# Optimization experiments

Measured on AMD Instinct MI355X. Metric: run time of the kernel, lower is better.

## Reference

```python
import jax, jax.numpy as jnp
import numpy as np

NUM_HEADS = 4
D_K = 64
D_MODEL = NUM_HEADS * D_K  # 256
SEN_LEN = 8192
N_GROUPS = 4096
BASE_LEN = 64
N_EDGES = N_GROUPS * BASE_LEN  # 262144
PATH_LEN = 64


def setup_inputs() -> dict:
    rng = np.random.default_rng(0)
    key = jax.random.key(0)
    ks = jax.random.split(key, 16)

    # ragged group lengths, each >= 2, summing exactly to N_EDGES
    half = N_GROUPS // 2
    r = rng.integers(-(BASE_LEN - 2), BASE_LEN - 1, size=half)
    edge_len = np.concatenate([BASE_LEN + r, BASE_LEN - r]).astype(np.int64)
    assert edge_len.sum() == N_EDGES and edge_len.min() >= 2

    # distinct token ids; include src=0 and tar=1 so path_agg branches fire
    perm = rng.permutation(np.arange(2, SEN_LEN))[: N_GROUPS - 2]
    token_ids = np.concatenate([np.array([0, 1]), perm]).astype(np.int64)

    def w(k, shape):
        return jax.random.normal(k, shape, jnp.float32) / np.sqrt(shape[-1]).astype(np.float32)

    return {
        "path": jax.random.normal(ks[0], (PATH_LEN, D_MODEL), jnp.float32),
        "path_len": PATH_LEN,
        "q": jax.random.normal(ks[1], (SEN_LEN, D_MODEL), jnp.float32),
        "k": jax.random.normal(ks[2], (N_EDGES, D_MODEL), jnp.float32),
        "v": jax.random.normal(ks[3], (N_EDGES, D_MODEL), jnp.float32),
        "graphs": 0,
        "edge_len": jnp.asarray(edge_len),
        "token_ids": jnp.asarray(token_ids),
        "pair": jnp.array([0, 1], jnp.int32),
        "rev": 0,
        "W_qpair": w(ks[4], (D_MODEL, 2 * D_MODEL)),
        "W_pk": w(ks[5], (D_MODEL, D_MODEL)),
        "W_pv": w(ks[6], (D_MODEL, D_MODEL)),
        "W_q": w(ks[7], (D_MODEL, D_MODEL)),
        "W_k": w(ks[8], (D_MODEL, D_MODEL)),
        "W_v": w(ks[9], (D_MODEL, D_MODEL)),
        "W_out": w(ks[10], (D_MODEL, D_MODEL)),
        "b_out": jnp.zeros((D_MODEL,), jnp.float32),
        "W_agg": w(ks[11], (D_MODEL, 2 * D_MODEL)),
    }


def _forward(path, q, k, v, edge_len, token_ids, pair, rev,
             W_qpair, W_pk, W_pv, W_q, W_k, W_v, W_out, b_out, W_agg):
    H, dk = NUM_HEADS, D_K
    G = edge_len.shape[0]
    E = k.shape[0]
    scale = 1.0 / jnp.sqrt(jnp.float32(dk))

    src = pair[0] if rev == 0 else pair[1]
    tar = pair[1] if rev == 0 else pair[0]

    # pair query: cat(q[src], q[tar]) -> linear -> [H, 1, dk]
    pair_q = (jnp.concatenate([q[src], q[tar]]) @ W_qpair.T).reshape(1, H, dk).transpose(1, 0, 2)

    qh = (q @ W_q.T).reshape(-1, H, dk).transpose(1, 0, 2)      # [H, S, dk]
    pk = (path @ W_pk.T).reshape(-1, H, dk).transpose(1, 0, 2)  # [H, P, dk]
    pv = (path @ W_pv.T).reshape(-1, H, dk).transpose(1, 0, 2)  # [H, P, dk]
    kh = (k @ W_k.T).reshape(-1, H, dk).transpose(1, 0, 2)      # [H, E, dk]
    vh = (v @ W_v.T).reshape(-1, H, dk).transpose(1, 0, 2)      # [H, E, dk]

    # ---- pair/path attention ----
    att = jax.nn.softmax(jnp.einsum('hqd,hpd->hqp', pair_q, pk) * scale, axis=-1)  # [H,1,P]
    path_vals = jnp.einsum('hqp,hpd->hqd', att, pv).sum(axis=1)  # [H, dk]
    path_result = path_vals.reshape(-1) @ W_out.T + b_out        # [d_model]

    # ---- segmented per-group attention (vectorized ragged loop) ----
    seg = jnp.repeat(jnp.arange(G), edge_len, total_repeat_length=E)  # [E]
    q_sel = qh[:, token_ids, :]          # [H, G, dk] query per group
    qe = q_sel[:, seg, :]                # [H, E, dk] query per edge
    # torch.matmul(q_[H,dk], k_[H,i,dk].T) broadcasts to cross-head logits [a,b,i]
    logits = jnp.einsum('aed,bed->eab', qe, kh) * scale  # [E, H, H]
    lmax = jax.lax.stop_gradient(jax.ops.segment_max(logits, seg, num_segments=G))
    ex = jnp.exp(logits - lmax[seg])
    denom = jax.ops.segment_sum(ex, seg, num_segments=G)
    p = ex / denom[seg]                                   # segmented softmax [E, H, H]
    # sum over key-head b per edge, then segment-reduce over edges of each group
    out_e = jnp.einsum('eab,bed->ead', p, vh)             # [E, H, dk]
    hid = jax.ops.segment_sum(out_e, seg, num_segments=G) # [G, H, dk]
    new_hid = hid.reshape(G, H * dk) @ W_out.T + b_out    # [G, d_model] (dropout=identity)

    # ---- assemble output rows ----
    pr = jnp.broadcast_to(path_result, (G, D_MODEL))
    feat_path = jnp.concatenate([new_hid, pr], axis=1) @ W_agg.T  # token == src
    path_feat = jnp.concatenate([pr, new_hid], axis=1) @ W_agg.T  # token == tar
    is_src = (token_ids == src)[:, None]
    is_tar = (token_ids == tar)[:, None]
    vals = jnp.where(is_src, feat_path, jnp.where(is_tar, path_feat, new_hid))
    returned = q.at[token_ids].set(vals)
    return returned, att


def reference(path, path_len, q, k, v, graphs, edge_len, token_ids, pair, rev,
              W_qpair, W_pk, W_pv, W_q, W_k, W_v, W_out, b_out, W_agg):
    return _forward(path, q, k, v, edge_len, token_ids, pair, rev,
                    W_qpair, W_pk, W_pv, W_q, W_k, W_v, W_out, b_out, W_agg)
```

## Files before the change

### kernel.cpp

```cpp
#include <hip/hip_runtime.h>
#include <hip/hip_bf16.h>

#define H 4
#define DK 64
#define DM 256
#define SEN 8192
#define NG 4096
#define ETOT 262144
#define PLEN 64
#define MAXE 128

typedef unsigned short ushortT;
typedef __attribute__((ext_vector_type(8))) __bf16 bf16x8;
typedef __attribute__((ext_vector_type(8))) unsigned short us8;
typedef __attribute__((ext_vector_type(4))) unsigned short us4;
typedef __attribute__((ext_vector_type(4))) float f32x4;

#define TMS 264

__device__ __forceinline__ ushortT f2bf(float f) {
    unsigned u = __float_as_uint(f);
    u += 0x7FFF + ((u >> 16) & 1);
    return (ushortT)(u >> 16);
}

__device__ __forceinline__ bf16x8 ldb8(const ushortT* p) {
    us8 v = *(const us8*)p;
    return __builtin_bit_cast(bf16x8, v);
}

__device__ __forceinline__ bf16x8 pack8(const float* f) {
    us8 v;
#pragma unroll
    for (int j = 0; j < 8; j++) v[j] = f2bf(f[j]);
    return __builtin_bit_cast(bf16x8, v);
}

__global__ __launch_bounds__(256) void scan_kernel(const int* __restrict__ edge_len,
                                                   int* __restrict__ starts) {
    __shared__ int part[256];
    const int tid = threadIdx.x;
    const int base = tid * 16;
    int loc[16];
    int s = 0;
#pragma unroll
    for (int i = 0; i < 16; i++) { loc[i] = s; s += edge_len[base + i]; }
    part[tid] = s;
    __syncthreads();
    if (tid == 0) {
        int acc = 0;
        for (int i = 0; i < 256; i++) { int t = part[i]; part[i] = acc; acc += t; }
    }
    __syncthreads();
    const int off = part[tid];
#pragma unroll
    for (int i = 0; i < 16; i++) starts[base + i] = off + loc[i];
}

__global__ void copy_kernel(const float* __restrict__ q, float* __restrict__ out) {
    const size_t i = (size_t)blockIdx.x * blockDim.x + threadIdx.x;
    ((float4*)out)[i] = ((const float4*)q)[i];
}

__global__ __launch_bounds__(256) void wprep_kernel(
    const float* __restrict__ W_q, const float* __restrict__ W_k,
    const float* __restrict__ W_v, const float* __restrict__ W_out,
    ushortT* __restrict__ WQb, ushortT* __restrict__ WKTb,
    ushortT* __restrict__ WVb, ushortT* __restrict__ WOb) {
    const int idx = blockIdx.x * 256 + threadIdx.x;
    const int sel = idx >> 16;
    const int i = idx & 65535;
    if (sel == 0) {
        WQb[i] = f2bf(W_q[i]);
    } else if (sel == 1) {
        const int c = i >> 8, d = i & 255;
        WKTb[i] = f2bf(W_k[d * DM + c]);
    } else if (sel == 2) {
        WVb[i] = f2bf(W_v[i]);
    } else {
        WOb[i] = f2bf(W_out[i]);
    }
}

__global__ __launch_bounds__(256) void qh_kernel(
    const float* __restrict__ q, const int* __restrict__ token_ids,
    const ushortT* __restrict__ WQb, ushortT* __restrict__ QHb) {
    __shared__ ushortT Al[64 * 264];
    const int tid = threadIdx.x;
    const int g0 = blockIdx.x * 64;
    {
        const int m = tid >> 2;
        const int c0 = (tid & 3) * 64;
        const int tok = token_ids[g0 + m];
        const float* qr = &q[(size_t)tok * DM + c0];
#pragma unroll
        for (int i = 0; i < 16; i++) {
            float4 v4 = *(const float4*)&qr[i * 4];
            us4 o;
            o[0] = f2bf(v4.x); o[1] = f2bf(v4.y); o[2] = f2bf(v4.z); o[3] = f2bf(v4.w);
            *(us4*)&Al[m * 264 + c0 + i * 4] = o;
        }
    }
    __syncthreads();
    const int lane = tid & 63, w = tid >> 6, lq = lane & 15, lh = lane >> 4;
    bf16x8 af[8];
#pragma unroll
    for (int kk = 0; kk < 8; kk++)
        af[kk] = ldb8(&Al[(w * 16 + lq) * 264 + kk * 32 + lh * 8]);
    for (int nt = 0; nt < 16; nt++) {
        f32x4 acc = {0.f, 0.f, 0.f, 0.f};
#pragma unroll
        for (int kk = 0; kk < 8; kk++) {
            bf16x8 bf = ldb8(&WQb[(nt * 16 + lq) * 256 + kk * 32 + lh * 8]);
            acc = __builtin_amdgcn_mfma_f32_16x16x32_bf16(af[kk], bf, acc, 0, 0, 0);
        }
#pragma unroll
        for (int r = 0; r < 4; r++)
            QHb[(size_t)(g0 + w * 16 + lh * 4 + r) * 256 + nt * 16 + lq] = f2bf(acc[r]);
    }
}

__global__ __launch_bounds__(256) void tmat_kernel(
    const ushortT* __restrict__ QHb, const ushortT* __restrict__ WKTb,
    ushortT* __restrict__ tmat_u) {
    const int tid = threadIdx.x;
    const int g0 = blockIdx.x * 64;
    const int ab = blockIdx.y;
    const int a = ab >> 2, b = ab & 3;
    const int lane = tid & 63, w = tid >> 6, lq = lane & 15, lh = lane >> 4;
    bf16x8 a0 = ldb8(&QHb[(size_t)(g0 + w * 16 + lq) * 256 + a * 64 + lh * 8]);
    bf16x8 a1 = ldb8(&QHb[(size_t)(g0 + w * 16 + lq) * 256 + a * 64 + 32 + lh * 8]);
    for (int nt = 0; nt < 16; nt++) {
        f32x4 acc = {0.f, 0.f, 0.f, 0.f};
        bf16x8 b0 = ldb8(&WKTb[(nt * 16 + lq) * 256 + b * 64 + lh * 8]);
        acc = __builtin_amdgcn_mfma_f32_16x16x32_bf16(a0, b0, acc, 0, 0, 0);
        bf16x8 b1 = ldb8(&WKTb[(nt * 16 + lq) * 256 + b * 64 + 32 + lh * 8]);
        acc = __builtin_amdgcn_mfma_f32_16x16x32_bf16(a1, b1, acc, 0, 0, 0);
#pragma unroll
        for (int r = 0; r < 4; r++)
            tmat_u[((size_t)(g0 + w * 16 + lh * 4 + r) * 16 + ab) * 256 + nt * 16 + lq] =
                f2bf(acc[r]);
    }
}

__global__ __launch_bounds__(256) void edge_kernel(
    const float* __restrict__ k, const float* __restrict__ v,
    const int* __restrict__ edge_len, const int* __restrict__ starts,
    ushortT* __restrict__ tmat_u) {
    const int g = blockIdx.x;
    const int tid = threadIdx.x;
    const float scale = 0.125f;
    __shared__ float plog[128][17];
    __shared__ ushortT pT[16 * 136];
    __shared__ float red[16][16];
    __shared__ float mx[16];
    const int start = starts[g];
    const int len = edge_len[g];
    const int lane = tid & 63, w = tid >> 6, lq = lane & 15, lh = lane >> 4;
    const int rg = tid >> 4, cc = tid & 15;

    bf16x8 btm[8];
#pragma unroll
    for (int cb = 0; cb < 8; cb++)
        btm[cb] = ldb8(&tmat_u[((size_t)g * 16 + lq) * 256 + cb * 32 + lh * 8]);

    const int nmt = (len + 15) >> 4;
    for (int t = w; t < nmt; t += 4) {
        const int e = t * 16 + lq;
        const int ec = (e < len) ? e : (len - 1);
        const float* krow = &k[(size_t)(start + ec) * DM + lh * 8];
        f32x4 acc = {0.f, 0.f, 0.f, 0.f};
#pragma unroll
        for (int cb = 0; cb < 8; cb++) {
            float4 k0 = *(const float4*)&krow[cb * 32];
            float4 k1 = *(const float4*)&krow[cb * 32 + 4];
            float kf[8] = {k0.x, k0.y, k0.z, k0.w, k1.x, k1.y, k1.z, k1.w};
            acc = __builtin_amdgcn_mfma_f32_16x16x32_bf16(pack8(kf), btm[cb], acc, 0, 0, 0);
        }
#pragma unroll
        for (int r = 0; r < 4; r++) plog[t * 16 + lh * 4 + r][lq] = acc[r] * scale;
    }
    __syncthreads();

    const int nkc = (len + 31) >> 5;
    {
        float m = -3.0e38f;
        for (int e = rg; e < len; e += 16) m = fmaxf(m, plog[e][cc]);
        red[rg][cc] = m;
        __syncthreads();
        if (tid < 16) {
            float mm = red[0][tid];
            for (int i2 = 1; i2 < 16; i2++) mm = fmaxf(mm, red[i2][tid]);
            mx[tid] = mm;
        }
        __syncthreads();
        const float mm = mx[cc];
        float s = 0.f;
        for (int e = rg; e < len; e += 16) {
            float ex = __expf(plog[e][cc] - mm);
            plog[e][cc] = ex;
            s += ex;
        }
        red[rg][cc] = s;
        __syncthreads();
        if (tid < 16) {
            float ss = red[0][tid];
            for (int i2 = 1; i2 < 16; i2++) ss += red[i2][tid];
            mx[tid] = 1.0f / ss;
        }
        __syncthreads();
        const float inv = mx[cc];
        const int padlen = nkc * 32;
        for (int e = rg; e < padlen; e += 16) {
            float pv = (e < len) ? plog[e][cc] * inv : 0.f;
            pT[cc * 136 + e] = f2bf(pv);
        }
    }
    __syncthreads();

    {
        f32x4 uacc[4];
#pragma unroll
        for (int nt = 0; nt < 4; nt++) uacc[nt] = {0.f, 0.f, 0.f, 0.f};
        const int c0 = w * 64;
#pragma unroll
        for (int kc = 0; kc < 4; kc++) {
            if (kc < nkc) {
                bf16x8 ap = ldb8(&pT[lq * 136 + kc * 32 + lh * 8]);
#pragma unroll
                for (int nt = 0; nt < 4; nt++) {
                    float bf[8];
#pragma unroll
                    for (int j = 0; j < 8; j++) {
                        int e = kc * 32 + lh * 8 + j;
                        int ecl = (e < len) ? e : (len - 1);
                        bf[j] = v[(size_t)(start + ecl) * DM + c0 + nt * 16 + lq];
                    }
                    uacc[nt] = __builtin_amdgcn_mfma_f32_16x16x32_bf16(ap, pack8(bf), uacc[nt], 0, 0, 0);
                }
            }
        }
#pragma unroll
        for (int nt = 0; nt < 4; nt++) {
#pragma unroll
            for (int r = 0; r < 4; r++) {
                const int ab = lh * 4 + r;
                tmat_u[((size_t)g * 16 + ab) * 256 + c0 + nt * 16 + lq] = f2bf(uacc[nt][r]);
            }
        }
    }
}

__global__ __launch_bounds__(256) void hid_kernel(
    const ushortT* __restrict__ Ub, const ushortT* __restrict__ WVb,
    ushortT* __restrict__ HIDb) {
    const int tid = threadIdx.x;
    const int g0 = blockIdx.x * 64;
    const int a = blockIdx.y;
    const int lane = tid & 63, w = tid >> 6, lq = lane & 15, lh = lane >> 4;
    f32x4 acc[4];
#pragma unroll
    for (int nt = 0; nt < 4; nt++) acc[nt] = {0.f, 0.f, 0.f, 0.f};
    for (int kk = 0; kk < 32; kk++) {
        const int kbase = kk * 32 + lh * 8;
        bf16x8 af = ldb8(&Ub[((size_t)(g0 + w * 16 + lq) * 16 + a * 4) * 256 + kbase]);
#pragma unroll
        for (int nt = 0; nt < 4; nt++) {
            bf16x8 bf = ldb8(&WVb[(size_t)((kbase >> 8) * 64 + nt * 16 + lq) * 256 + (kbase & 255)]);
            acc[nt] = __builtin_amdgcn_mfma_f32_16x16x32_bf16(af, bf, acc[nt], 0, 0, 0);
        }
    }
#pragma unroll
    for (int nt = 0; nt < 4; nt++) {
#pragma unroll
        for (int r = 0; r < 4; r++)
            HIDb[(size_t)(g0 + w * 16 + lh * 4 + r) * 256 + a * 64 + nt * 16 + lq] =
                f2bf(acc[nt][r]);
    }
}

__global__ __launch_bounds__(256) void nh_kernel(
    const ushortT* __restrict__ HIDb, const ushortT* __restrict__ WOb,
    const float* __restrict__ b_out, const int* __restrict__ token_ids,
    float* __restrict__ nh_ws, float* __restrict__ out) {
    const int tid = threadIdx.x;
    const int g0 = blockIdx.x * 64;
    const int lane = tid & 63, w = tid >> 6, lq = lane & 15, lh = lane >> 4;
    bf16x8 af[8];
#pragma unroll
    for (int kk = 0; kk < 8; kk++)
        af[kk] = ldb8(&HIDb[(size_t)(g0 + w * 16 + lq) * 256 + kk * 32 + lh * 8]);
    int toks[4];
#pragma unroll
    for (int r = 0; r < 4; r++) toks[r] = token_ids[g0 + w * 16 + lh * 4 + r];
    for (int nt = 0; nt < 16; nt++) {
        f32x4 acc = {0.f, 0.f, 0.f, 0.f};
#pragma unroll
        for (int kk = 0; kk < 8; kk++) {
            bf16x8 bf = ldb8(&WOb[(nt * 16 + lq) * 256 + kk * 32 + lh * 8]);
            acc = __builtin_amdgcn_mfma_f32_16x16x32_bf16(af[kk], bf, acc, 0, 0, 0);
        }
        const int n = nt * 16 + lq;
        const float bo = b_out[n];
#pragma unroll
        for (int r = 0; r < 4; r++) {
            const int g = g0 + w * 16 + lh * 4 + r;
            const float val = acc[r] + bo;
            nh_ws[(size_t)g * 256 + n] = val;
            out[(size_t)toks[r] * DM + n] = val;
        }
    }
}

__global__ __launch_bounds__(256) void agg_kernel(
    const int* __restrict__ token_ids, const int* __restrict__ pair,
    const int* __restrict__ rev, const float* __restrict__ W_agg,
    const float* __restrict__ path_result, const float* __restrict__ nh_ws,
    float* __restrict__ out) {
    __shared__ int gsrc, gtar;
    __shared__ float catS[512], catT[512];
    const int tid = threadIdx.x;
    if (tid == 0) { gsrc = -1; gtar = -1; }
    __syncthreads();
    const int rv = rev[0];
    const int src = (rv == 0) ? pair[0] : pair[1];
    const int tar = (rv == 0) ? pair[1] : pair[0];
    for (int i = tid; i < NG; i += 256) {
        const int tk = token_ids[i];
        if (tk == src) gsrc = i;
        if (tk == tar) gtar = i;
    }
    __syncthreads();
    const int gs = gsrc, gt = gtar;
    if (gs >= 0) {
        catS[tid] = nh_ws[(size_t)gs * 256 + tid];
        catS[256 + tid] = path_result[tid];
    }
    if (gt >= 0) {
        catT[tid] = path_result[tid];
        catT[256 + tid] = nh_ws[(size_t)gt * 256 + tid];
    }
    __syncthreads();
    if (gs >= 0) {
        float acc = 0.f;
        for (int n = 0; n < 512; n += 4) {
            float4 w4 = *(const float4*)&W_agg[(size_t)tid * 512 + n];
            acc += w4.x * catS[n] + w4.y * catS[n + 1] + w4.z * catS[n + 2] + w4.w * catS[n + 3];
        }
        out[(size_t)src * DM + tid] = acc;
    }
    if (gt >= 0) {
        float acc = 0.f;
        for (int n = 0; n < 512; n += 4) {
            float4 w4 = *(const float4*)&W_agg[(size_t)tid * 512 + n];
            acc += w4.x * catT[n] + w4.y * catT[n + 1] + w4.z * catT[n + 2] + w4.w * catT[n + 3];
        }
        out[(size_t)tar * DM + tid] = acc;
    }
}

__global__ __launch_bounds__(256) void pathB_kernel(
    const float* __restrict__ path, const float* __restrict__ q,
    const int* __restrict__ pair, const int* __restrict__ rev,
    const float* __restrict__ W_qpair, const float* __restrict__ W_pk,
    const float* __restrict__ W_pv,
    float* __restrict__ pv_ws, float* __restrict__ logits_ws) {
    __shared__ float cat[512];
    __shared__ float pq[256];
    __shared__ float prow[256];
    __shared__ float lp[256];
    const int p = blockIdx.x;
    const int tid = threadIdx.x;
    const int rv = rev[0];
    const int src = (rv == 0) ? pair[0] : pair[1];
    const int tar = (rv == 0) ? pair[1] : pair[0];
    cat[tid] = q[(size_t)src * DM + tid];
    cat[256 + tid] = q[(size_t)tar * DM + tid];
    prow[tid] = path[p * DM + tid];
    __syncthreads();
    float acc = 0.f;
    for (int c = 0; c < 512; c += 4) {
        float4 w4 = *(const float4*)&W_qpair[(size_t)tid * 512 + c];
        acc += w4.x * cat[c] + w4.y * cat[c + 1] + w4.z * cat[c + 2] + w4.w * cat[c + 3];
    }
    pq[tid] = acc;
    __syncthreads();
    float pkv = 0.f, pvv = 0.f;
    for (int c = 0; c < 256; c += 4) {
        float4 a4 = *(const float4*)&W_pk[tid * DM + c];
        float4 b4 = *(const float4*)&W_pv[tid * DM + c];
        float4 x4 = *(const float4*)&prow[c];
        pkv += a4.x * x4.x + a4.y * x4.y + a4.z * x4.z + a4.w * x4.w;
        pvv += b4.x * x4.x + b4.y * x4.y + b4.z * x4.z + b4.w * x4.w;
    }
    pv_ws[p * DM + tid] = pvv;
    lp[tid] = pq[tid] * pkv;
    __syncthreads();
    if (tid < H) {
        float s = 0.f;
        for (int d = 0; d < DK; d++) s += lp[tid * DK + d];
        logits_ws[tid * PLEN + p] = s * 0.125f;
    }
}

__global__ __launch_bounds__(256) void pathC_kernel(
    const float* __restrict__ pv_ws, const float* __restrict__ logits_ws,
    const float* __restrict__ W_out, const float* __restrict__ b_out,
    float* __restrict__ att_out, float* __restrict__ path_result) {
    __shared__ float att[256];
    __shared__ float pvals[256];
    const int tid = threadIdx.x;
    att[tid] = logits_ws[tid];
    __syncthreads();
    if (tid < H) {
        float m = -3.0e38f;
        for (int p = 0; p < PLEN; p++) m = fmaxf(m, att[tid * PLEN + p]);
        float s = 0.f;
        for (int p = 0; p < PLEN; p++) {
            float e = __expf(att[tid * PLEN + p] - m);
            att[tid * PLEN + p] = e;
            s += e;
        }
        float inv = 1.f / s;
        for (int p = 0; p < PLEN; p++) att[tid * PLEN + p] *= inv;
    }
    __syncthreads();
    att_out[tid] = att[tid];
    {
        const int h = tid >> 6;
        float a = 0.f;
        for (int p = 0; p < PLEN; p++) a += att[h * PLEN + p] * pv_ws[p * DM + tid];
        pvals[tid] = a;
    }
    __syncthreads();
    {
        float a = b_out[tid];
        for (int c = 0; c < 256; c += 4) {
            float4 w4 = *(const float4*)&W_out[tid * DM + c];
            a += w4.x * pvals[c] + w4.y * pvals[c + 1] + w4.z * pvals[c + 2] + w4.w * pvals[c + 3];
        }
        path_result[tid] = a;
    }
}

__global__ __launch_bounds__(256, 4) void group_kernel(
    const float* __restrict__ q, const float* __restrict__ k, const float* __restrict__ v,
    const int* __restrict__ edge_len, const int* __restrict__ token_ids,
    const int* __restrict__ pair, const int* __restrict__ rev,
    const float* __restrict__ W_q,
    const float* __restrict__ W_k, const float* __restrict__ W_v,
    const float* __restrict__ W_out, const float* __restrict__ b_out,
    const float* __restrict__ W_agg,
    const int* __restrict__ starts, const float* __restrict__ path_result,
    float* __restrict__ out) {
    const int g = blockIdx.x;
    const int tid = threadIdx.x;
    const float scale = 0.125f;

    __shared__ float qrow[256];
    __shared__ float qh[256];
    __shared__ ushortT qh_b[4 * 72];
    __shared__ ushortT tmat_b[16 * TMS];
    __shared__ float plog[128][17];
    __shared__ ushortT pT[16 * 136];
    __shared__ ushortT u_b[4 * 1032];
    __shared__ float hid[256];
    __shared__ float nh[256];
    __shared__ float red[16][16];
    __shared__ float mx[16];

    const int tok = token_ids[g];
    const int start = starts[g];
    const int len = edge_len[g];

    const int lane = tid & 63;
    const int w = tid >> 6;
    const int lq = lane & 15;
    const int lh = lane >> 4;
    const int rg = tid >> 4;
    const int cc = tid & 15;

    qrow[tid] = q[(size_t)tok * DM + tid];
    __syncthreads();

    for (int i = 0; i < 16; i++) {
        const int r = i * 16 + rg;
        float acc = 0.f;
#pragma unroll
        for (int j4 = 0; j4 < 4; j4++) {
            const int c0 = j4 * 64 + cc * 4;
            float4 w4 = *(const float4*)&W_q[r * DM + c0];
            float4 x4 = *(const float4*)&qrow[c0];
            acc += w4.x * x4.x + w4.y * x4.y + w4.z * x4.z + w4.w * x4.w;
        }
#pragma unroll
        for (int off = 8; off; off >>= 1) acc += __shfl_down(acc, off, 16);
        if (cc == 0) qh[r] = acc;
    }
    __syncthreads();
    qh_b[(tid >> 6) * 72 + (tid & 63)] = f2bf(qh[tid]);
    __syncthreads();

    {
        const int arow = (lq < 3) ? lq : 3;
        bf16x8 aq0 = ldb8(&qh_b[arow * 72 + lh * 8]);
        bf16x8 aq1 = ldb8(&qh_b[arow * 72 + 32 + lh * 8]);
        for (int nt = 0; nt < 16; nt++) {
            const int c = nt * 16 + lq;
            f32x4 acc = {0.f, 0.f, 0.f, 0.f};
            float wf[8];
#pragma unroll
            for (int j = 0; j < 8; j++)
                wf[j] = W_k[(size_t)(w * 64 + lh * 8 + j) * DM + c];
            acc = __builtin_amdgcn_mfma_f32_16x16x32_bf16(aq0, pack8(wf), acc, 0, 0, 0);
#pragma unroll
            for (int j = 0; j < 8; j++)
                wf[j] = W_k[(size_t)(w * 64 + 32 + lh * 8 + j) * DM + c];
            acc = __builtin_amdgcn_mfma_f32_16x16x32_bf16(aq1, pack8(wf), acc, 0, 0, 0);
            if (lane < 16) {
#pragma unroll
                for (int r = 0; r < 4; r++)
                    tmat_b[(r * 4 + w) * TMS + nt * 16 + lq] = f2bf(acc[r]);
            }
        }
    }
    __syncthreads();

    {
        bf16x8 btm[8];
#pragma unroll
        for (int cb = 0; cb < 8; cb++)
            btm[cb] = ldb8(&tmat_b[lq * TMS + cb * 32 + lh * 8]);
        const int nmt = (len + 15) >> 4;
        for (int t = w; t < nmt; t += 4) {
            const int e = t * 16 + lq;
            const int ec = (e < len) ? e : (len - 1);
            const float* krow = &k[(size_t)(start + ec) * DM + lh * 8];
            f32x4 acc = {0.f, 0.f, 0.f, 0.f};
#pragma unroll
            for (int cb = 0; cb < 8; cb++) {
                float4 k0 = *(const float4*)&krow[cb * 32];
                float4 k1 = *(const float4*)&krow[cb * 32 + 4];
                float kf[8] = {k0.x, k0.y, k0.z, k0.w, k1.x, k1.y, k1.z, k1.w};
                acc = __builtin_amdgcn_mfma_f32_16x16x32_bf16(pack8(kf), btm[cb], acc, 0, 0, 0);
            }
#pragma unroll
            for (int r = 0; r < 4; r++) plog[t * 16 + lh * 4 + r][lq] = acc[r] * scale;
        }
    }
    __syncthreads();

    const int nkc = (len + 31) >> 5;
    {
        float m = -3.0e38f;
        for (int e = rg; e < len; e += 16) m = fmaxf(m, plog[e][cc]);
        red[rg][cc] = m;
        __syncthreads();
        if (tid < 16) {
            float mm = red[0][tid];
            for (int i2 = 1; i2 < 16; i2++) mm = fmaxf(mm, red[i2][tid]);
            mx[tid] = mm;
        }
        __syncthreads();
        const float mm = mx[cc];
        float s = 0.f;
        for (int e = rg; e < len; e += 16) {
            float ex = __expf(plog[e][cc] - mm);
            plog[e][cc] = ex;
            s += ex;
        }
        red[rg][cc] = s;
        __syncthreads();
        if (tid < 16) {
            float ss = red[0][tid];
            for (int i2 = 1; i2 < 16; i2++) ss += red[i2][tid];
            mx[tid] = 1.0f / ss;
        }
        __syncthreads();
        const float inv = mx[cc];
        const int padlen = nkc * 32;
        for (int e = rg; e < padlen; e += 16) {
            float pv = (e < len) ? plog[e][cc] * inv : 0.f;
            pT[cc * 136 + e] = f2bf(pv);
        }
    }
    __syncthreads();

    {
        f32x4 uacc[4];
#pragma unroll
        for (int nt = 0; nt < 4; nt++) uacc[nt] = {0.f, 0.f, 0.f, 0.f};
        const int c0 = w * 64;
#pragma unroll
        for (int kc = 0; kc < 4; kc++) {
            if (kc < nkc) {
                bf16x8 ap = ldb8(&pT[lq * 136 + kc * 32 + lh * 8]);
#pragma unroll
                for (int nt = 0; nt < 4; nt++) {
                    float bf[8];
#pragma unroll
                    for (int j = 0; j < 8; j++) {
                        int e = kc * 32 + lh * 8 + j;
                        int ecl = (e < len) ? e : (len - 1);
                        bf[j] = v[(size_t)(start + ecl) * DM + c0 + nt * 16 + lq];
                    }
                    uacc[nt] = __builtin_amdgcn_mfma_f32_16x16x32_bf16(ap, pack8(bf), uacc[nt], 0, 0, 0);
                }
            }
        }
#pragma unroll
        for (int nt = 0; nt < 4; nt++) {
#pragma unroll
            for (int r = 0; r < 4; r++) {
                const int row = lh * 4 + r;
                const int a = row >> 2, b = row & 3;
                u_b[a * 1032 + b * 256 + c0 + nt * 16 + lq] = f2bf(uacc[nt][r]);
            }
        }
    }
    __syncthreads();

    {
        const int arow = (lq < 3) ? lq : 3;
        f32x4 hacc = {0.f, 0.f, 0.f, 0.f};
        for (int kc = 0; kc < 32; kc++) {
            bf16x8 au = ldb8(&u_b[arow * 1032 + kc * 32 + lh * 8]);
            const int kk = kc * 32 + lh * 8;
            const float* wr = &W_v[(size_t)((kk >> 8) * 64 + w * 16 + lq) * DM + (kk & 255)];
            float4 w0 = *(const float4*)&wr[0];
            float4 w1 = *(const float4*)&wr[4];
            float wf[8] = {w0.x, w0.y, w0.z, w0.w, w1.x, w1.y, w1.z, w1.w};
            hacc = __builtin_amdgcn_mfma_f32_16x16x32_bf16(au, pack8(wf), hacc, 0, 0, 0);
        }
        if (lane < 16) {
#pragma unroll
            for (int r = 0; r < 4; r++) hid[r * 64 + w * 16 + lq] = hacc[r];
        }
    }
    __syncthreads();

    for (int i = 0; i < 16; i++) {
        const int m = i * 16 + rg;
        float acc = 0.f;
#pragma unroll
        for (int j4 = 0; j4 < 4; j4++) {
            const int c0 = j4 * 64 + cc * 4;
            float4 w4 = *(const float4*)&W_out[m * DM + c0];
            float4 h4 = *(const float4*)&hid[c0];
            acc += w4.x * h4.x + w4.y * h4.y + w4.z * h4.z + w4.w * h4.w;
        }
#pragma unroll
        for (int off = 8; off; off >>= 1) acc += __shfl_down(acc, off, 16);
        if (cc == 0) nh[m] = b_out[m] + acc;
    }
    __syncthreads();

    const int rv = rev[0];
    const int src = (rv == 0) ? pair[0] : pair[1];
    const int tar = (rv == 0) ? pair[1] : pair[0];
    float val;
    if (tok == src || tok == tar) {
        qrow[tid] = path_result[tid];
        __syncthreads();
        const float* x1 = (tok == src) ? nh : qrow;
        const float* x2 = (tok == src) ? qrow : nh;
        float acc = 0.f;
        for (int n = 0; n < 256; n += 4) {
            float4 w4 = *(const float4*)&W_agg[(size_t)tid * 512 + n];
            acc += w4.x * x1[n] + w4.y * x1[n + 1] + w4.z * x1[n + 2] + w4.w * x1[n + 3];
        }
        for (int n = 0; n < 256; n += 4) {
            float4 w4 = *(const float4*)&W_agg[(size_t)tid * 512 + 256 + n];
            acc += w4.x * x2[n] + w4.y * x2[n + 1] + w4.z * x2[n + 2] + w4.w * x2[n + 3];
        }
        val = acc;
    } else {
        val = nh[tid];
    }
    out[(size_t)tok * DM + tid] = val;
}

extern "C" void kernel_launch(void* const* d_in, const int* in_sizes, int n_in,
                              void* d_out, int out_size, void* d_ws, size_t ws_size,
                              hipStream_t stream) {
    const float* path    = (const float*)d_in[0];
    const float* q       = (const float*)d_in[2];
    const float* k       = (const float*)d_in[3];
    const float* v       = (const float*)d_in[4];
    const int*   edge_len  = (const int*)d_in[6];
    const int*   token_ids = (const int*)d_in[7];
    const int*   pair      = (const int*)d_in[8];
    const int*   rev       = (const int*)d_in[9];
    const float* W_qpair = (const float*)d_in[10];
    const float* W_pk    = (const float*)d_in[11];
    const float* W_pv    = (const float*)d_in[12];
    const float* W_q     = (const float*)d_in[13];
    const float* W_k     = (const float*)d_in[14];
    const float* W_v     = (const float*)d_in[15];
    const float* W_out   = (const float*)d_in[16];
    const float* b_out   = (const float*)d_in[17];
    const float* W_agg   = (const float*)d_in[18];
    float* out = (float*)d_out;

    char* base = (char*)d_ws;
    int*    starts      = (int*)(base + 0);
    float*  path_result = (float*)(base + 16384);
    float*  pv_ws       = (float*)(base + 17408);
    float*  logits_ws   = (float*)(base + 82944);
    float*  nh_ws       = (float*)(base + 83968);
    ushortT* QHb        = (ushortT*)(base + 4278272);
    ushortT* HIDb       = (ushortT*)(base + 6375424);
    ushortT* WQb        = (ushortT*)(base + 8472576);
    ushortT* WKTb       = (ushortT*)(base + 8603648);
    ushortT* WVb        = (ushortT*)(base + 8734720);
    ushortT* WOb        = (ushortT*)(base + 8865792);
    ushortT* tmat_u     = (ushortT*)(base + 8996864);
    const size_t NEED = 42551296;

    copy_kernel<<<dim3(2048), dim3(256), 0, stream>>>(q, out);
    scan_kernel<<<dim3(1), dim3(256), 0, stream>>>(edge_len, starts);
    pathB_kernel<<<dim3(PLEN), dim3(256), 0, stream>>>(path, q, pair, rev, W_qpair, W_pk,
                                                       W_pv, pv_ws, logits_ws);
    pathC_kernel<<<dim3(1), dim3(256), 0, stream>>>(pv_ws, logits_ws, W_out, b_out,
                                                    out + (size_t)SEN * DM, path_result);

    if (ws_size >= NEED) {
        wprep_kernel<<<dim3(1024), dim3(256), 0, stream>>>(W_q, W_k, W_v, W_out,
                                                           WQb, WKTb, WVb, WOb);
        qh_kernel<<<dim3(64), dim3(256), 0, stream>>>(q, token_ids, WQb, QHb);
        tmat_kernel<<<dim3(64, 16), dim3(256), 0, stream>>>(QHb, WKTb, tmat_u);
        edge_kernel<<<dim3(NG), dim3(256), 0, stream>>>(k, v, edge_len, starts, tmat_u);
        hid_kernel<<<dim3(64, 4), dim3(256), 0, stream>>>(tmat_u, WVb, HIDb);
        nh_kernel<<<dim3(64), dim3(256), 0, stream>>>(HIDb, WOb, b_out, token_ids,
                                                      nh_ws, out);
        agg_kernel<<<dim3(1), dim3(256), 0, stream>>>(token_ids, pair, rev, W_agg,
                                                      path_result, nh_ws, out);
    } else {
        group_kernel<<<dim3(NG), dim3(256), 0, stream>>>(q, k, v, edge_len, token_ids, pair,
                                                         rev, W_q, W_k, W_v, W_out, b_out,
                                                         W_agg, starts, path_result, out);
    }
}
```

Baseline: 320.4 us.

## Fuse qh+tmat and hid+nh kernels, stage V through LDS with prefetch

Merges the Q-head projection and tmat computation into one kernel that keeps QH in shared memory, and merges hid and nh into one kernel that keeps HID in shared memory. This removes the QHb, HIDb and nh_ws workspace round trips and two launches; agg now reads new_hid back from out. In edge_kernel, V rows are loaded with coalesced float4 reads into an LDS buffer, and the next chunk is prefetched into registers, replacing strided scalar gathers. Bf16 conversion now uses native casts instead of manual rounding. The fused kernels use smaller 16-group tiles and add extra LDS use in edge_kernel, which may reduce occupancy.

```diff
diff --git a/kernel.cpp b/kernel.cpp
--- a/kernel.cpp
+++ b/kernel.cpp
@@ -23,17 +23,24 @@
     u += 0x7FFF + ((u >> 16) & 1);
     return (ushortT)(u >> 16);
 }
-
 __device__ __forceinline__ bf16x8 ldb8(const ushortT* p) {
     us8 v = *(const us8*)p;
     return __builtin_bit_cast(bf16x8, v);
 }
-
 __device__ __forceinline__ bf16x8 pack8(const float* f) {
     us8 v;
 #pragma unroll
     for (int j = 0; j < 8; j++) v[j] = f2bf(f[j]);
     return __builtin_bit_cast(bf16x8, v);
+}
+__device__ __forceinline__ ushortT sbf(float f) {
+    return __builtin_bit_cast(ushortT, (__bf16)f);
+}
+__device__ __forceinline__ bf16x8 pack8f(float4 a, float4 b) {
+    bf16x8 r;
+    r[0] = (__bf16)a.x; r[1] = (__bf16)a.y; r[2] = (__bf16)a.z; r[3] = (__bf16)a.w;
+    r[4] = (__bf16)b.x; r[5] = (__bf16)b.y; r[6] = (__bf16)b.z; r[7] = (__bf16)b.w;
+    return r;
 }
 
 __global__ __launch_bounds__(256) void scan_kernel(const int* __restrict__ edge_len,
@@ -71,75 +78,76 @@
     const int sel = idx >> 16;
     const int i = idx & 65535;
     if (sel == 0) {
-        WQb[i] = f2bf(W_q[i]);
+        WQb[i] = sbf(W_q[i]);
     } else if (sel == 1) {
         const int c = i >> 8, d = i & 255;
-        WKTb[i] = f2bf(W_k[d * DM + c]);
+        WKTb[i] = sbf(W_k[d * DM + c]);
     } else if (sel == 2) {
-        WVb[i] = f2bf(W_v[i]);
+        WVb[i] = sbf(W_v[i]);
     } else {
-        WOb[i] = f2bf(W_out[i]);
-    }
-}
-
-__global__ __launch_bounds__(256) void qh_kernel(
+        WOb[i] = sbf(W_out[i]);
+    }
+}
+
+__global__ __launch_bounds__(256) void qhtmat_kernel(
     const float* __restrict__ q, const int* __restrict__ token_ids,
-    const ushortT* __restrict__ WQb, ushortT* __restrict__ QHb) {
-    __shared__ ushortT Al[64 * 264];
+    const ushortT* __restrict__ WQb, const ushortT* __restrict__ WKTb,
+    ushortT* __restrict__ tmat_u) {
+    __shared__ ushortT Al[16 * 264];
+    __shared__ ushortT QHs[16 * 264];
     const int tid = threadIdx.x;
-    const int g0 = blockIdx.x * 64;
-    {
-        const int m = tid >> 2;
-        const int c0 = (tid & 3) * 64;
+    const int g0 = blockIdx.x * 16;
+    const int lane = tid & 63, w = tid >> 6, lq = lane & 15, lh = lane >> 4;
+    {
+        const int m = tid >> 4;
+        const int c0 = (tid & 15) * 16;
         const int tok = token_ids[g0 + m];
         const float* qr = &q[(size_t)tok * DM + c0];
 #pragma unroll
-        for (int i = 0; i < 16; i++) {
+        for (int i = 0; i < 4; i++) {
             float4 v4 = *(const float4*)&qr[i * 4];
             us4 o;
-            o[0] = f2bf(v4.x); o[1] = f2bf(v4.y); o[2] = f2bf(v4.z); o[3] = f2bf(v4.w);
+            o[0] = sbf(v4.x); o[1] = sbf(v4.y); o[2] = sbf(v4.z); o[3] = sbf(v4.w);
             *(us4*)&Al[m * 264 + c0 + i * 4] = o;
         }
     }
     __syncthreads();
-    const int lane = tid & 63, w = tid >> 6, lq = lane & 15, lh = lane >> 4;
-    bf16x8 af[8];
-#pragma unroll
-    for (int kk = 0; kk < 8; kk++)
-        af[kk] = ldb8(&Al[(w * 16 + lq) * 264 + kk * 32 + lh * 8]);
-    for (int nt = 0; nt < 16; nt++) {
-        f32x4 acc = {0.f, 0.f, 0.f, 0.f};
-#pragma unroll
-        for (int kk = 0; kk < 8; kk++) {
-            bf16x8 bf = ldb8(&WQb[(nt * 16 + lq) * 256 + kk * 32 + lh * 8]);
-            acc = __builtin_amdgcn_mfma_f32_16x16x32_bf16(af[kk], bf, acc, 0, 0, 0);
-        }
-#pragma unroll
-        for (int r = 0; r < 4; r++)
-            QHb[(size_t)(g0 + w * 16 + lh * 4 + r) * 256 + nt * 16 + lq] = f2bf(acc[r]);
-    }
-}
-
-__global__ __launch_bounds__(256) void tmat_kernel(
-    const ushortT* __restrict__ QHb, const ushortT* __restrict__ WKTb,
-    ushortT* __restrict__ tmat_u) {
-    const int tid = threadIdx.x;
-    const int g0 = blockIdx.x * 64;
-    const int ab = blockIdx.y;
-    const int a = ab >> 2, b = ab & 3;
-    const int lane = tid & 63, w = tid >> 6, lq = lane & 15, lh = lane >> 4;
-    bf16x8 a0 = ldb8(&QHb[(size_t)(g0 + w * 16 + lq) * 256 + a * 64 + lh * 8]);
-    bf16x8 a1 = ldb8(&QHb[(size_t)(g0 + w * 16 + lq) * 256 + a * 64 + 32 + lh * 8]);
-    for (int nt = 0; nt < 16; nt++) {
-        f32x4 acc = {0.f, 0.f, 0.f, 0.f};
-        bf16x8 b0 = ldb8(&WKTb[(nt * 16 + lq) * 256 + b * 64 + lh * 8]);
-        acc = __builtin_amdgcn_mfma_f32_16x16x32_bf16(a0, b0, acc, 0, 0, 0);
-        bf16x8 b1 = ldb8(&WKTb[(nt * 16 + lq) * 256 + b * 64 + 32 + lh * 8]);
-        acc = __builtin_amdgcn_mfma_f32_16x16x32_bf16(a1, b1, acc, 0, 0, 0);
-#pragma unroll
-        for (int r = 0; r < 4; r++)
-            tmat_u[((size_t)(g0 + w * 16 + lh * 4 + r) * 16 + ab) * 256 + nt * 16 + lq] =
-                f2bf(acc[r]);
+    {
+        bf16x8 af[8];
+#pragma unroll
+        for (int kk = 0; kk < 8; kk++) af[kk] = ldb8(&Al[lq * 264 + kk * 32 + lh * 8]);
+#pragma unroll
+        for (int ntl = 0; ntl < 4; ntl++) {
+            const int nt = w * 4 + ntl;
+            f32x4 acc = {0.f, 0.f, 0.f, 0.f};
+#pragma unroll
+            for (int kk = 0; kk < 8; kk++) {
+                bf16x8 bf = ldb8(&WQb[(nt * 16 + lq) * 256 + kk * 32 + lh * 8]);
+                acc = __builtin_amdgcn_mfma_f32_16x16x32_bf16(af[kk], bf, acc, 0, 0, 0);
+            }
+#pragma unroll
+            for (int r = 0; r < 4; r++)
+                QHs[(lh * 4 + r) * 264 + nt * 16 + lq] = sbf(acc[r]);
+        }
+    }
+    __syncthreads();
+    for (int ab = 0; ab < 16; ab++) {
+        const int a = ab >> 2, b = ab & 3;
+        bf16x8 a0 = ldb8(&QHs[lq * 264 + a * 64 + lh * 8]);
+        bf16x8 a1 = ldb8(&QHs[lq * 264 + a * 64 + 32 + lh * 8]);
+#pragma unroll
+        for (int ntl = 0; ntl < 4; ntl++) {
+            const int nt = w * 4 + ntl;
+            f32x4 acc = {0.f, 0.f, 0.f, 0.f};
+            bf16x8 b0 = ldb8(&WKTb[(nt * 16 + lq) * 256 + b * 64 + lh * 8]);
+            acc = __builtin_amdgcn_mfma_f32_16x16x32_bf16(a0, b0, acc, 0, 0, 0);
+            bf16x8 b1 = ldb8(&WKTb[(nt * 16 + lq) * 256 + b * 64 + 32 + lh * 8]);
+            acc = __builtin_amdgcn_mfma_f32_16x16x32_bf16(a1, b1, acc, 0, 0, 0);
+#pragma unroll
+            for (int r = 0; r < 4; r++)
+                tmat_u[((size_t)(g0 + lh * 4 + r) * 16 + ab) * 256 + nt * 16 + lq] =
+                    sbf(acc[r]);
+        }
     }
 }
 
@@ -154,10 +162,21 @@
     __shared__ ushortT pT[16 * 136];
     __shared__ float red[16][16];
     __shared__ float mx[16];
+    __shared__ float vbuf[32 * 258];
     const int start = starts[g];
     const int len = edge_len[g];
     const int lane = tid & 63, w = tid >> 6, lq = lane & 15, lh = lane >> 4;
     const int rg = tid >> 4, cc = tid & 15;
+    const int vrow = tid & 31, vcs = tid >> 5;
+    const int nkc = (len + 31) >> 5;
+
+    float4 vr[8];
+    {
+        const int ecl = (vrow < len) ? vrow : (len - 1);
+        const float* src = &v[(size_t)(start + ecl) * DM + vcs * 32];
+#pragma unroll
+        for (int i = 0; i < 8; i++) vr[i] = *(const float4*)&src[i * 4];
+    }
 
     bf16x8 btm[8];
 #pragma unroll
@@ -174,15 +193,13 @@
         for (int cb = 0; cb < 8; cb++) {
             float4 k0 = *(const float4*)&krow[cb * 32];
             float4 k1 = *(const float4*)&krow[cb * 32 + 4];
-            float kf[8] = {k0.x, k0.y, k0.z, k0.w, k1.x, k1.y, k1.z, k1.w};
-            acc = __builtin_amdgcn_mfma_f32_16x16x32_bf16(pack8(kf), btm[cb], acc, 0, 0, 0);
+            acc = __builtin_amdgcn_mfma_f32_16x16x32_bf16(pack8f(k0, k1), btm[cb], acc, 0, 0, 0);
         }
 #pragma unroll
         for (int r = 0; r < 4; r++) plog[t * 16 + lh * 4 + r][lq] = acc[r] * scale;
     }
     __syncthreads();
 
-    const int nkc = (len + 31) >> 5;
     {
         float m = -3.0e38f;
         for (int e = rg; e < len; e += 16) m = fmaxf(m, plog[e][cc]);
@@ -222,101 +239,93 @@
         f32x4 uacc[4];
 #pragma unroll
         for (int nt = 0; nt < 4; nt++) uacc[nt] = {0.f, 0.f, 0.f, 0.f};
+        const int wb = vrow * 258 + vcs * 32;
+        for (int kc = 0; kc < nkc; kc++) {
+#pragma unroll
+            for (int i = 0; i < 8; i++) {
+                *(float2*)&vbuf[wb + i * 4]     = make_float2(vr[i].x, vr[i].y);
+                *(float2*)&vbuf[wb + i * 4 + 2] = make_float2(vr[i].z, vr[i].w);
+            }
+            __syncthreads();
+            if (kc + 1 < nkc) {
+                const int e = (kc + 1) * 32 + vrow;
+                const int ecl = (e < len) ? e : (len - 1);
+                const float* src = &v[(size_t)(start + ecl) * DM + vcs * 32];
+#pragma unroll
+                for (int i = 0; i < 8; i++) vr[i] = *(const float4*)&src[i * 4];
+            }
+            bf16x8 ap = ldb8(&pT[lq * 136 + kc * 32 + lh * 8]);
+#pragma unroll
+            for (int nt = 0; nt < 4; nt++) {
+                bf16x8 bv;
+#pragma unroll
+                for (int j = 0; j < 8; j++)
+                    bv[j] = (__bf16)vbuf[(lh * 8 + j) * 258 + w * 64 + nt * 16 + lq];
+                uacc[nt] = __builtin_amdgcn_mfma_f32_16x16x32_bf16(ap, bv, uacc[nt], 0, 0, 0);
+            }
+            __syncthreads();
+        }
         const int c0 = w * 64;
-#pragma unroll
-        for (int kc = 0; kc < 4; kc++) {
-            if (kc < nkc) {
-                bf16x8 ap = ldb8(&pT[lq * 136 + kc * 32 + lh * 8]);
-#pragma unroll
-                for (int nt = 0; nt < 4; nt++) {
-                    float bf[8];
-#pragma unroll
-                    for (int j = 0; j < 8; j++) {
-                        int e = kc * 32 + lh * 8 + j;
-                        int ecl = (e < len) ? e : (len - 1);
-                        bf[j] = v[(size_t)(start + ecl) * DM + c0 + nt * 16 + lq];
-                    }
-                    uacc[nt] = __builtin_amdgcn_mfma_f32_16x16x32_bf16(ap, pack8(bf), uacc[nt], 0, 0, 0);
-                }
-            }
-        }
 #pragma unroll
         for (int nt = 0; nt < 4; nt++) {
 #pragma unroll
             for (int r = 0; r < 4; r++) {
                 const int ab = lh * 4 + r;
-                tmat_u[((size_t)g * 16 + ab) * 256 + c0 + nt * 16 + lq] = f2bf(uacc[nt][r]);
-            }
-        }
-    }
-}
-
-__global__ __launch_bounds__(256) void hid_kernel(
+                tmat_u[((size_t)g * 16 + ab) * 256 + c0 + nt * 16 + lq] = sbf(uacc[nt][r]);
+            }
+        }
+    }
+}
+
+__global__ __launch_bounds__(256) void hidnh_kernel(
     const ushortT* __restrict__ Ub, const ushortT* __restrict__ WVb,
-    ushortT* __restrict__ HIDb) {
+    const ushortT* __restrict__ WOb, const float* __restrict__ b_out,
+    const int* __restrict__ token_ids, float* __restrict__ out) {
+    __shared__ ushortT HIDs[16 * 264];
     const int tid = threadIdx.x;
-    const int g0 = blockIdx.x * 64;
-    const int a = blockIdx.y;
+    const int g0 = blockIdx.x * 16;
     const int lane = tid & 63, w = tid >> 6, lq = lane & 15, lh = lane >> 4;
-    f32x4 acc[4];
-#pragma unroll
-    for (int nt = 0; nt < 4; nt++) acc[nt] = {0.f, 0.f, 0.f, 0.f};
-    for (int kk = 0; kk < 32; kk++) {
-        const int kbase = kk * 32 + lh * 8;
-        bf16x8 af = ldb8(&Ub[((size_t)(g0 + w * 16 + lq) * 16 + a * 4) * 256 + kbase]);
-#pragma unroll
-        for (int nt = 0; nt < 4; nt++) {
-            bf16x8 bf = ldb8(&WVb[(size_t)((kbase >> 8) * 64 + nt * 16 + lq) * 256 + (kbase & 255)]);
-            acc[nt] = __builtin_amdgcn_mfma_f32_16x16x32_bf16(af, bf, acc[nt], 0, 0, 0);
-        }
-    }
-#pragma unroll
-    for (int nt = 0; nt < 4; nt++) {
+#pragma unroll
+    for (int a = 0; a < 4; a++) {
+        f32x4 acc = {0.f, 0.f, 0.f, 0.f};
+        for (int kk = 0; kk < 32; kk++) {
+            const int kbase = kk * 32 + lh * 8;
+            bf16x8 af = ldb8(&Ub[((size_t)(g0 + lq) * 16 + a * 4) * 256 + kbase]);
+            bf16x8 bf = ldb8(&WVb[(size_t)((kbase >> 8) * 64 + w * 16 + lq) * 256 + (kbase & 255)]);
+            acc = __builtin_amdgcn_mfma_f32_16x16x32_bf16(af, bf, acc, 0, 0, 0);
+        }
 #pragma unroll
         for (int r = 0; r < 4; r++)
-            HIDb[(size_t)(g0 + w * 16 + lh * 4 + r) * 256 + a * 64 + nt * 16 + lq] =
-                f2bf(acc[nt][r]);
-    }
-}
-
-__global__ __launch_bounds__(256) void nh_kernel(
-    const ushortT* __restrict__ HIDb, const ushortT* __restrict__ WOb,
-    const float* __restrict__ b_out, const int* __restrict__ token_ids,
-    float* __restrict__ nh_ws, float* __restrict__ out) {
-    const int tid = threadIdx.x;
-    const int g0 = blockIdx.x * 64;
-    const int lane = tid & 63, w = tid >> 6, lq = lane & 15, lh = lane >> 4;
-    bf16x8 af[8];
-#pragma unroll
-    for (int kk = 0; kk < 8; kk++)
-        af[kk] = ldb8(&HIDb[(size_t)(g0 + w * 16 + lq) * 256 + kk * 32 + lh * 8]);
+            HIDs[(lh * 4 + r) * 264 + a * 64 + w * 16 + lq] = sbf(acc[r]);
+    }
+    __syncthreads();
+    bf16x8 af2[8];
+#pragma unroll
+    for (int kk = 0; kk < 8; kk++) af2[kk] = ldb8(&HIDs[lq * 264 + kk * 32 + lh * 8]);
     int toks[4];
 #pragma unroll
-    for (int r = 0; r < 4; r++) toks[r] = token_ids[g0 + w * 16 + lh * 4 + r];
-    for (int nt = 0; nt < 16; nt++) {
+    for (int r = 0; r < 4; r++) toks[r] = token_ids[g0 + lh * 4 + r];
+#pragma unroll
+    for (int ntl = 0; ntl < 4; ntl++) {
+        const int nt = w * 4 + ntl;
         f32x4 acc = {0.f, 0.f, 0.f, 0.f};
 #pragma unroll
         for (int kk = 0; kk < 8; kk++) {
             bf16x8 bf = ldb8(&WOb[(nt * 16 + lq) * 256 + kk * 32 + lh * 8]);
-            acc = __builtin_amdgcn_mfma_f32_16x16x32_bf16(af[kk], bf, acc, 0, 0, 0);
+            acc = __builtin_amdgcn_mfma_f32_16x16x32_bf16(af2[kk], bf, acc, 0, 0, 0);
         }
         const int n = nt * 16 + lq;
         const float bo = b_out[n];
 #pragma unroll
-        for (int r = 0; r < 4; r++) {
-            const int g = g0 + w * 16 + lh * 4 + r;
-            const float val = acc[r] + bo;
-            nh_ws[(size_t)g * 256 + n] = val;
-            out[(size_t)toks[r] * DM + n] = val;
-        }
+        for (int r = 0; r < 4; r++)
+            out[(size_t)toks[r] * DM + n] = acc[r] + bo;
     }
 }
 
 __global__ __launch_bounds__(256) void agg_kernel(
     const int* __restrict__ token_ids, const int* __restrict__ pair,
     const int* __restrict__ rev, const float* __restrict__ W_agg,
-    const float* __restrict__ path_result, const float* __restrict__ nh_ws,
-    float* __restrict__ out) {
+    const float* __restrict__ path_result, float* __restrict__ out) {
     __shared__ int gsrc, gtar;
     __shared__ float catS[512], catT[512];
     const int tid = threadIdx.x;
@@ -333,12 +342,12 @@
     __syncthreads();
     const int gs = gsrc, gt = gtar;
     if (gs >= 0) {
-        catS[tid] = nh_ws[(size_t)gs * 256 + tid];
+        catS[tid] = out[(size_t)src * DM + tid];
         catS[256 + tid] = path_result[tid];
     }
     if (gt >= 0) {
         catT[tid] = path_result[tid];
-        catT[256 + tid] = nh_ws[(size_t)gt * 256 + tid];
+        catT[256 + tid] = out[(size_t)tar * DM + tid];
     }
     __syncthreads();
     if (gs >= 0) {
@@ -707,15 +716,12 @@
     float*  path_result = (float*)(base + 16384);
     float*  pv_ws       = (float*)(base + 17408);
     float*  logits_ws   = (float*)(base + 82944);
-    float*  nh_ws       = (float*)(base + 83968);
-    ushortT* QHb        = (ushortT*)(base + 4278272);
-    ushortT* HIDb       = (ushortT*)(base + 6375424);
-    ushortT* WQb        = (ushortT*)(base + 8472576);
-    ushortT* WKTb       = (ushortT*)(base + 8603648);
-    ushortT* WVb        = (ushortT*)(base + 8734720);
-    ushortT* WOb        = (ushortT*)(base + 8865792);
-    ushortT* tmat_u     = (ushortT*)(base + 8996864);
-    const size_t NEED = 42551296;
+    ushortT* WQb        = (ushortT*)(base + 83968);
+    ushortT* WKTb       = (ushortT*)(base + 215040);
+    ushortT* WVb        = (ushortT*)(base + 346112);
+    ushortT* WOb        = (ushortT*)(base + 477184);
+    ushortT* tmat_u     = (ushortT*)(base + 608256);
+    const size_t NEED = 608256 + 33554432;
 
     copy_kernel<<<dim3(2048), dim3(256), 0, stream>>>(q, out);
     scan_kernel<<<dim3(1), dim3(256), 0, stream>>>(edge_len, starts);
@@ -727,14 +733,12 @@
     if (ws_size >= NEED) {
         wprep_kernel<<<dim3(1024), dim3(256), 0, stream>>>(W_q, W_k, W_v, W_out,
                                                            WQb, WKTb, WVb, WOb);
-        qh_kernel<<<dim3(64), dim3(256), 0, stream>>>(q, token_ids, WQb, QHb);
-        tmat_kernel<<<dim3(64, 16), dim3(256), 0, stream>>>(QHb, WKTb, tmat_u);
+        qhtmat_kernel<<<dim3(256), dim3(256), 0, stream>>>(q, token_ids, WQb, WKTb, tmat_u);
         edge_kernel<<<dim3(NG), dim3(256), 0, stream>>>(k, v, edge_len, starts, tmat_u);
-        hid_kernel<<<dim3(64, 4), dim3(256), 0, stream>>>(tmat_u, WVb, HIDb);
-        nh_kernel<<<dim3(64), dim3(256), 0, stream>>>(HIDb, WOb, b_out, token_ids,
-                                                      nh_ws, out);
+        hidnh_kernel<<<dim3(256), dim3(256), 0, stream>>>(tmat_u, WVb, WOb, b_out,
+                                                          token_ids, out);
         agg_kernel<<<dim3(1), dim3(256), 0, stream>>>(token_ids, pair, rev, W_agg,
-                                                      path_result, nh_ws, out);
+                                                      path_result, out);
     } else {
         group_kernel<<<dim3(NG), dim3(256), 0, stream>>>(q, k, v, edge_len, token_ids, pair,
                                                          rev, W_q, W_k, W_v, W_out, b_out,
```

Result: faster. 300.8 us (-6.1%).
